# Kernel optimization log

Measured on AMD Instinct MI355X. Metric: run time of the kernel, lower is better.

The kernel has to match this reference:

```python
import jax, jax.numpy as jnp
import numpy as np

B, T, C, H = 4, 2048, 768, 12
D = C // H
EPS = 1e-5


def layernorm(x, g, b):
    mu = jnp.mean(x, axis=-1, keepdims=True)
    var = jnp.mean(jnp.square(x - mu), axis=-1, keepdims=True)
    return (x - mu) * jax.lax.rsqrt(var + EPS) * g + b


def setup_inputs() -> dict:
    key = jax.random.key(0)
    ks = jax.random.split(key, 16)
    s = 0.02
    return {
        "x": jax.random.normal(ks[0], (B, T, C), jnp.float32),
        "Wq": jax.random.normal(ks[1], (C, C), jnp.float32) * s,
        "bq": jnp.zeros((C,), jnp.float32),
        "Wk": jax.random.normal(ks[2], (C, C), jnp.float32) * s,
        "bk": jnp.zeros((C,), jnp.float32),
        "Wv": jax.random.normal(ks[3], (C, C), jnp.float32) * s,
        "bv": jnp.zeros((C,), jnp.float32),
        "Wo": jax.random.normal(ks[4], (C, C), jnp.float32) * s,
        "bo": jnp.zeros((C,), jnp.float32),
        "g1": jnp.ones((C,), jnp.float32),
        "b1": jnp.zeros((C,), jnp.float32),
        "g2": jnp.ones((C,), jnp.float32),
        "b2": jnp.zeros((C,), jnp.float32),
        "W1": jax.random.normal(ks[5], (C, 4 * C), jnp.float32) * s,
        "bm1": jnp.zeros((4 * C,), jnp.float32),
        "W2": jax.random.normal(ks[6], (4 * C, C), jnp.float32) * s,
        "bm2": jnp.zeros((C,), jnp.float32),
    }


def reference(x, Wq, bq, Wk, bk, Wv, bv, Wo, bo, g1, b1, g2, b2, W1, bm1, W2, bm2):
    # --- attention branch ---
    h = layernorm(x, g1, b1)
    q = (h @ Wq + bq).reshape(B, T, H, D)
    k = (h @ Wk + bk).reshape(B, T, H, D)
    v = (h @ Wv + bv).reshape(B, T, H, D)
    att = jnp.einsum('bqhd,bkhd->bhqk', q, k) / jnp.sqrt(jnp.float32(D))
    causal = jnp.tril(jnp.ones((T, T), bool))
    att = jnp.where(causal, att, -jnp.inf)
    att = jax.nn.softmax(att, axis=-1)
    o = jnp.einsum('bhqk,bkhd->bqhd', att, v).reshape(B, T, C)
    x = x + o @ Wo + bo
    # --- MLP branch ---
    h = layernorm(x, g2, b2)
    h = jax.nn.gelu(h @ W1 + bm1, approximate=False)
    return x + h @ W2 + bm2
```

## Files before the change

kernel.cpp:

```cpp
#include <hip/hip_runtime.h>
#include <hip/hip_bf16.h>

#define B_ 4
#define T_ 2048
#define C_ 768
#define H_ 12
#define D_ 64
#define QS_ 2304

typedef __attribute__((ext_vector_type(8))) short short8;
typedef __attribute__((ext_vector_type(4))) short short4v;
typedef __attribute__((ext_vector_type(4))) float f32x4;

__device__ __forceinline__ unsigned short f2bf(float f) {
    __hip_bfloat16 h = __float2bfloat16(f);
    return *reinterpret_cast<unsigned short*>(&h);
}

__device__ __forceinline__ float bf2f(unsigned short u) {
    return __bfloat162float(*reinterpret_cast<const __hip_bfloat16*>(&u));
}

__device__ __forceinline__ unsigned cvt_pk_bf16(float lo, float hi) {
    unsigned r;
    asm("v_cvt_pk_bf16_f32 %0, %1, %2" : "=v"(r) : "v"(lo), "v"(hi));
    return r;
}

__device__ __forceinline__ void gl_lds16(const void* g, void* l) {
    __builtin_amdgcn_global_load_lds((const __attribute__((address_space(1))) unsigned int*)g,
                                     (__attribute__((address_space(3))) unsigned int*)l,
                                     16, 0, 0);
}

__device__ __forceinline__ void transpose_dev(const float* __restrict__ W,
                                              unsigned short* __restrict__ Wt,
                                              int K, int N, int bx, int by,
                                              float (*t)[65]) {
    int n0 = bx * 64, k0 = by * 64;
    int r = threadIdx.x >> 4, c4 = (threadIdx.x & 15) * 4;
    #pragma unroll
    for (int i = 0; i < 4; ++i) {
        float4 v = *(const float4*)(W + (size_t)(k0 + i * 16 + r) * N + n0 + c4);
        t[i*16 + r][c4 + 0] = v.x;
        t[i*16 + r][c4 + 1] = v.y;
        t[i*16 + r][c4 + 2] = v.z;
        t[i*16 + r][c4 + 3] = v.w;
    }
    __syncthreads();
    #pragma unroll
    for (int i = 0; i < 4; ++i) {
        ushort4 o;
        o.x = f2bf(t[c4 + 0][i*16 + r]);
        o.y = f2bf(t[c4 + 1][i*16 + r]);
        o.z = f2bf(t[c4 + 2][i*16 + r]);
        o.w = f2bf(t[c4 + 3][i*16 + r]);
        *(ushort4*)(Wt + (size_t)(n0 + i * 16 + r) * K + k0 + c4) = o;
    }
}

__global__ __launch_bounds__(256) void prep_all(const float* __restrict__ Wq,
                                                const float* __restrict__ Wk,
                                                const float* __restrict__ Wv,
                                                const float* __restrict__ Wo,
                                                const float* __restrict__ W1,
                                                const float* __restrict__ W2,
                                                const float* __restrict__ bq,
                                                const float* __restrict__ bk,
                                                const float* __restrict__ bv,
                                                const float* __restrict__ x,
                                                const float* __restrict__ g1,
                                                const float* __restrict__ b1,
                                                unsigned short* __restrict__ wqkvt,
                                                unsigned short* __restrict__ wot,
                                                unsigned short* __restrict__ w1t,
                                                unsigned short* __restrict__ w2t,
                                                float* __restrict__ bqkv,
                                                unsigned short* __restrict__ ln1h) {
    __shared__ float t[64][65];
    int blk = blockIdx.x;
    int tid = threadIdx.x;

    if (blk < 576) {
        int which = blk / 144, idx = blk % 144;
        const float* src = (which == 0) ? Wq : (which == 1) ? Wk : (which == 2) ? Wv : Wo;
        unsigned short* dst = (which == 3) ? wot : wqkvt + (size_t)which * C_ * C_;
        transpose_dev(src, dst, C_, C_, idx % 12, idx / 12, t);
    } else if (blk < 1152) {
        int idx = blk - 576;
        transpose_dev(W1, w1t, C_, 4 * C_, idx % 48, idx / 48, t);
    } else if (blk < 1728) {
        int idx = blk - 1152;
        transpose_dev(W2, w2t, 4 * C_, C_, idx % 12, idx / 12, t);
    } else if (blk < 1737) {
        int i = (blk - 1728) * 256 + tid;
        bqkv[i] = (i < 768) ? bq[i] : (i < 1536) ? bk[i - 768] : bv[i - 1536];
    } else {
        int row = (blk - 1737) * 4 + (tid >> 6);
        int lane = tid & 63;
        const float* xr = x + (size_t)row * C_;
        float v[12];
        #pragma unroll
        for (int p = 0; p < 3; ++p) {
            float4 f4 = *(const float4*)(xr + p * 256 + lane * 4);
            v[p*4+0] = f4.x; v[p*4+1] = f4.y; v[p*4+2] = f4.z; v[p*4+3] = f4.w;
        }
        float s = 0.f;
        #pragma unroll
        for (int i = 0; i < 12; ++i) s += v[i];
        #pragma unroll
        for (int off = 1; off < 64; off <<= 1) s += __shfl_xor(s, off);
        float mean = s * (1.0f / C_);
        float qs = 0.f;
        #pragma unroll
        for (int i = 0; i < 12; ++i) { v[i] -= mean; qs += v[i] * v[i]; }
        #pragma unroll
        for (int off = 1; off < 64; off <<= 1) qs += __shfl_xor(qs, off);
        float rs = rsqrtf(qs * (1.0f / C_) + 1e-5f);
        unsigned short* orow = ln1h + (size_t)row * C_;
        #pragma unroll
        for (int p = 0; p < 3; ++p) {
            float4 gv = *(const float4*)(g1 + p * 256 + lane * 4);
            float4 bv = *(const float4*)(b1 + p * 256 + lane * 4);
            ushort4 o4;
            o4.x = f2bf(v[p*4+0] * rs * gv.x + bv.x);
            o4.y = f2bf(v[p*4+1] * rs * gv.y + bv.y);
            o4.z = f2bf(v[p*4+2] * rs * gv.z + bv.z);
            o4.w = f2bf(v[p*4+3] * rs * gv.w + bv.w);
            *(ushort4*)(orow + p * 256 + lane * 4) = o4;
        }
    }
}

__global__ __launch_bounds__(256) void ln2_wave(const unsigned short* __restrict__ x,
                                                const float* __restrict__ g,
                                                const float* __restrict__ b,
                                                unsigned short* __restrict__ out) {
    int row = blockIdx.x * 4 + (threadIdx.x >> 6);
    int lane = threadIdx.x & 63;
    const unsigned short* xr = x + (size_t)row * C_;
    float v[12];
    #pragma unroll
    for (int p = 0; p < 3; ++p) {
        ushort4 u4 = *(const ushort4*)(xr + p * 256 + lane * 4);
        v[p*4+0] = bf2f(u4.x); v[p*4+1] = bf2f(u4.y);
        v[p*4+2] = bf2f(u4.z); v[p*4+3] = bf2f(u4.w);
    }
    float s = 0.f;
    #pragma unroll
    for (int i = 0; i < 12; ++i) s += v[i];
    #pragma unroll
    for (int off = 1; off < 64; off <<= 1) s += __shfl_xor(s, off);
    float mean = s * (1.0f / C_);
    float qs = 0.f;
    #pragma unroll
    for (int i = 0; i < 12; ++i) { v[i] -= mean; qs += v[i] * v[i]; }
    #pragma unroll
    for (int off = 1; off < 64; off <<= 1) qs += __shfl_xor(qs, off);
    float rs = rsqrtf(qs * (1.0f / C_) + 1e-5f);
    unsigned short* orow = out + (size_t)row * C_;
    #pragma unroll
    for (int p = 0; p < 3; ++p) {
        float4 gv = *(const float4*)(g + p * 256 + lane * 4);
        float4 bv = *(const float4*)(b + p * 256 + lane * 4);
        ushort4 o4;
        o4.x = f2bf(v[p*4+0] * rs * gv.x + bv.x);
        o4.y = f2bf(v[p*4+1] * rs * gv.y + bv.y);
        o4.z = f2bf(v[p*4+2] * rs * gv.z + bv.z);
        o4.w = f2bf(v[p*4+3] * rs * gv.w + bv.w);
        *(ushort4*)(orow + p * 256 + lane * 4) = o4;
    }
}

template <int EPI>
__global__ __launch_bounds__(256) void gemm_bf16(const unsigned short* __restrict__ A,
                                                 const unsigned short* __restrict__ Bt,
                                                 const float* __restrict__ bias,
                                                 const void* __restrict__ resid,
                                                 void* __restrict__ Cout,
                                                 unsigned short* __restrict__ aux,
                                                 int M, int N, int K, int gx) {
    __shared__ short As[2][128 * 32];
    __shared__ short Bs[2][128 * 32];
    int tid = threadIdx.x;
    int w = tid >> 6, l = tid & 63;
    int nb = gridDim.x;
    int per = nb >> 3;
    int fid = (int)blockIdx.x;
    int wid = (fid & 7) * per + (fid >> 3);
    int bn = wid % gx, bm = wid / gx;
    int wr = w >> 1, wc = w & 1;

    f32x4 acc[4][4];
    #pragma unroll
    for (int m = 0; m < 4; ++m)
        #pragma unroll
        for (int n = 0; n < 4; ++n)
            acc[m][n] = (f32x4){0.f, 0.f, 0.f, 0.f};

    const short* Ag = (const short*)A + (size_t)(bm * 128) * K;
    const short* Bg = (const short*)Bt + (size_t)(bn * 128) * K;
    int srow = tid >> 2;
    int scol = (tid & 3) * 8;
    int lrow = l & 15, lk = (l >> 4) * 8;

    auto stage = [&](int buf, int k0) {
        #pragma unroll
        for (int i = 0; i < 2; ++i) {
            gl_lds16(Ag + (size_t)(i * 64 + srow) * K + k0 + scol,
                     (char*)&As[buf][0] + i * 4096 + w * 1024);
            gl_lds16(Bg + (size_t)(i * 64 + srow) * K + k0 + scol,
                     (char*)&Bs[buf][0] + i * 4096 + w * 1024);
        }
    };

    int nk = K / 32;
    stage(0, 0);
    __syncthreads();

    for (int kt = 0; kt < nk; ++kt) {
        int cur = kt & 1;
        if (kt + 1 < nk) stage(cur ^ 1, (kt + 1) * 32);

        short8 av[4], bv[4];
        #pragma unroll
        for (int m = 0; m < 4; ++m)
            av[m] = *(const short8*)&As[cur][(wr * 64 + m * 16 + lrow) * 32 + lk];
        #pragma unroll
        for (int n = 0; n < 4; ++n)
            bv[n] = *(const short8*)&Bs[cur][(wc * 64 + n * 16 + lrow) * 32 + lk];
        #pragma unroll
        for (int m = 0; m < 4; ++m)
            #pragma unroll
            for (int n = 0; n < 4; ++n)
                acc[m][n] = __builtin_amdgcn_mfma_f32_16x16x32_bf16(av[m], bv[n], acc[m][n], 0, 0, 0);

        __syncthreads();
    }

    int lcol = l & 15, lr4 = (l >> 4) * 4;
    int row0 = bm * 128 + wr * 64;
    int col0 = bn * 128 + wc * 64;
    #pragma unroll
    for (int m = 0; m < 4; ++m) {
        #pragma unroll
        for (int n = 0; n < 4; ++n) {
            int col = col0 + n * 16 + lcol;
            float bz = bias[col];
            if (EPI == 5 && col0 >= 1536) {
                ushort4 o4;
                o4.x = f2bf(acc[m][n][0] + bz);
                o4.y = f2bf(acc[m][n][1] + bz);
                o4.z = f2bf(acc[m][n][2] + bz);
                o4.w = f2bf(acc[m][n][3] + bz);
                int row = row0 + m * 16 + lr4;
                int c = col - 1536;
                *(ushort4*)(aux + ((size_t)(row >> 11) * 768 + c) * (size_t)T_ + (row & 2047)) = o4;
            } else {
                #pragma unroll
                for (int r = 0; r < 4; ++r) {
                    int row = row0 + m * 16 + lr4 + r;
                    float v = acc[m][n][r] + bz;
                    if (EPI == 1) {
                        float u = fmaf(0.044715f * v, v * v, v);
                        float e = __builtin_amdgcn_exp2f(u * -2.3022127f);
                        v = v * __builtin_amdgcn_rcpf(1.0f + e);
                        ((unsigned short*)Cout)[(size_t)row * N + col] = f2bf(v);
                    } else if (EPI == 6) {
                        v += bf2f(((const unsigned short*)resid)[(size_t)row * N + col]);
                        ((float*)Cout)[(size_t)row * N + col] = v;
                    } else if (EPI == 7) {
                        v += ((const float*)resid)[(size_t)row * N + col];
                        ((unsigned short*)Cout)[(size_t)row * N + col] = f2bf(v);
                    } else {
                        ((unsigned short*)Cout)[(size_t)row * N + col] = f2bf(v);
                    }
                }
            }
        }
    }
}

__global__ __launch_bounds__(256) void attn_v9(const unsigned short* __restrict__ QKV,
                                               const unsigned short* __restrict__ vT,
                                               unsigned short* __restrict__ O) {
    __shared__ short Ks[128 * 64];
    __shared__ short Vt[64 * 128];

    int tid = threadIdx.x;
    int w = tid >> 6, l = tid & 63;
    int g = l >> 4, lc = l & 15;
    int wid = (int)(blockIdx.x & 7) * 192 + (int)(blockIdx.x >> 3);
    int bh = wid >> 5;
    int a  = 31 - (wid & 31);
    int b = bh / H_, h = bh % H_;
    const size_t bT = (size_t)b * T_;
    const unsigned short* Qp = QKV + h * D_;
    const unsigned short* Kp = QKV + 768 + h * D_;
    const unsigned short* vTb = vT + ((size_t)b * 768 + h * 64) * (size_t)T_;
    const float SCL = 0.125f * 1.44269504088896340736f;

    int qw = a * 64 + w * 16;

    short8 qf[2];
    {
        const unsigned short* qp = Qp + (bT + qw + lc) * QS_;
        qf[0] = *(const short8*)(qp + g * 8);
        qf[1] = *(const short8*)(qp + 32 + g * 8);
    }

    f32x4 oacc[4];
    #pragma unroll
    for (int n = 0; n < 4; ++n) oacc[n] = (f32x4){0.f, 0.f, 0.f, 0.f};
    float mrun = 4.0f, lpart = 0.f;

    int ntiles = (a >> 1) + 1;
    for (int kt = 0; kt < ntiles; ++kt) {
        int k0 = kt * 128;
        if (kt) __syncthreads();

        #pragma unroll
        for (int c = 0; c < 4; ++c) {
            int row = w * 32 + c * 8 + (l >> 3);
            int inner = (l & 7) * 16;
            const char* src = (const char*)(Kp + (bT + k0 + row) * QS_)
                              + (inner ^ ((row & 7) << 4));
            gl_lds16(src, (char*)Ks + w * 4096 + c * 1024);
        }
        #pragma unroll
        for (int c = 0; c < 4; ++c) {
            int d = w * 16 + c * 4 + (l >> 4);
            int inner = (l & 15) * 16;
            const char* src = (const char*)(vTb + (size_t)d * T_ + k0)
                              + (inner ^ ((d & 7) << 4));
            gl_lds16(src, (char*)Vt + w * 4096 + c * 1024);
        }
        __syncthreads();

        uint2 qd[8];
        float lmaxP[4] = {-INFINITY, -INFINITY, -INFINITY, -INFINITY};
        float rsumP[4] = {0.f, 0.f, 0.f, 0.f};
        bool full = (k0 + 127 <= qw);
        #pragma unroll
        for (int mk = 0; mk < 8; ++mk) {
            f32x4 s = (f32x4){0.f, 0.f, 0.f, 0.f};
            __builtin_amdgcn_s_setprio(1);
            #pragma unroll
            for (int ksd = 0; ksd < 2; ++ksd) {
                int row = mk * 16 + lc;
                int byt = (row * 128 + ksd * 64 + g * 16) ^ ((row & 7) << 4);
                short8 av = *(const short8*)((char*)Ks + byt);
                s = __builtin_amdgcn_mfma_f32_16x16x32_bf16(av, qf[ksd], s, 0, 0, 0);
            }
            __builtin_amdgcn_s_setprio(0);
            float p[4];
            #pragma unroll
            for (int r = 0; r < 4; ++r) {
                float sv = s[r] * SCL;
                if (!full && (k0 + mk * 16 + g * 4 + r > qw + lc)) sv = -INFINITY;
                lmaxP[r] = fmaxf(lmaxP[r], sv);
                float pv = __builtin_amdgcn_exp2f(sv - mrun);
                p[r] = pv;
                rsumP[r] += pv;
            }
            qd[mk].x = cvt_pk_bf16(p[0], p[1]);
            qd[mk].y = cvt_pk_bf16(p[2], p[3]);
        }
        float lmax = fmaxf(fmaxf(lmaxP[0], lmaxP[1]), fmaxf(lmaxP[2], lmaxP[3]));
        lpart += (rsumP[0] + rsumP[1]) + (rsumP[2] + rsumP[3]);

        #pragma unroll
        for (int ks = 0; ks < 4; ++ks) {
            uint2 qa = qd[ks * 2], qb = qd[ks * 2 + 1];
            int srcLo = lc + ((g & 1) << 5);
            int srcHi = srcLo + 16;
            unsigned a0 = (unsigned)__shfl((int)qa.x, srcLo);
            unsigned a1 = (unsigned)__shfl((int)qa.y, srcLo);
            unsigned a2 = (unsigned)__shfl((int)qa.x, srcHi);
            unsigned a3 = (unsigned)__shfl((int)qa.y, srcHi);
            unsigned b0 = (unsigned)__shfl((int)qb.x, srcLo);
            unsigned b1 = (unsigned)__shfl((int)qb.y, srcLo);
            unsigned b2 = (unsigned)__shfl((int)qb.x, srcHi);
            unsigned b3 = (unsigned)__shfl((int)qb.y, srcHi);
            bool lo = (g < 2);
            union { unsigned u[4]; short8 s8; } pa;
            pa.u[0] = lo ? a0 : b0;
            pa.u[1] = lo ? a1 : b1;
            pa.u[2] = lo ? a2 : b2;
            pa.u[3] = lo ? a3 : b3;
            short8 vbv[4];
            #pragma unroll
            for (int n = 0; n < 4; ++n) {
                int row = n * 16 + lc;
                int byt = (row * 256 + ks * 64 + g * 16) ^ ((row & 7) << 4);
                vbv[n] = *(const short8*)((char*)Vt + byt);
            }
            __builtin_amdgcn_s_setprio(1);
            #pragma unroll
            for (int n = 0; n < 4; ++n)
                oacc[n] = __builtin_amdgcn_mfma_f32_16x16x32_bf16(pa.s8, vbv[n], oacc[n], 0, 0, 0);
            __builtin_amdgcn_s_setprio(0);
        }

        if (__any(lmax > mrun + 8.0f)) {
            lmax = fmaxf(lmax, __shfl_xor(lmax, 16));
            lmax = fmaxf(lmax, __shfl_xor(lmax, 32));
            float mnew = fmaxf(mrun, lmax);
            float cc = __builtin_amdgcn_exp2f(mrun - mnew);
            lpart *= cc;
            mrun = mnew;
            #pragma unroll
            for (int r = 0; r < 4; ++r) {
                float cr = __shfl(cc, (l & 48) + g * 4 + r);
                #pragma unroll
                for (int n = 0; n < 4; ++n) oacc[n][r] *= cr;
            }
        }
    }

    float lv = lpart;
    lv += __shfl_xor(lv, 16);
    lv += __shfl_xor(lv, 32);
    float linv = 1.0f / lv;
    float inv[4];
    #pragma unroll
    for (int r = 0; r < 4; ++r) inv[r] = __shfl(linv, (l & 48) + g * 4 + r);
    #pragma unroll
    for (int n = 0; n < 4; ++n) {
        int col = h * D_ + n * 16 + lc;
        #pragma unroll
        for (int r = 0; r < 4; ++r) {
            int row = qw + g * 4 + r;
            O[(bT + row) * C_ + col] = f2bf(oacc[n][r] * inv[r]);
        }
    }
}

extern "C" void kernel_launch(void* const* d_in, const int* in_sizes, int n_in,
                              void* d_out, int out_size, void* d_ws, size_t ws_size,
                              hipStream_t stream) {
    const float* x   = (const float*)d_in[0];
    const float* Wq  = (const float*)d_in[1];
    const float* bq  = (const float*)d_in[2];
    const float* Wk  = (const float*)d_in[3];
    const float* bk  = (const float*)d_in[4];
    const float* Wv  = (const float*)d_in[5];
    const float* bv  = (const float*)d_in[6];
    const float* Wo  = (const float*)d_in[7];
    const float* bo  = (const float*)d_in[8];
    const float* g1  = (const float*)d_in[9];
    const float* b1  = (const float*)d_in[10];
    const float* g2  = (const float*)d_in[11];
    const float* b2  = (const float*)d_in[12];
    const float* W1  = (const float*)d_in[13];
    const float* bm1 = (const float*)d_in[14];
    const float* W2  = (const float*)d_in[15];
    const float* bm2 = (const float*)d_in[16];
    float* out = (float*)d_out;

    const size_t S = (size_t)B_ * T_ * C_;
    char* base = (char*)d_ws;
    unsigned short* ln1h = (unsigned short*)base;
    unsigned short* qkvb = (unsigned short*)(base + 2 * S);
    unsigned short* o    = ln1h;
    unsigned short* ln2h = qkvb;
    unsigned short* vT   = (unsigned short*)(base + 8 * S);
    unsigned short* hid  = (unsigned short*)(base + 4 * S);
    unsigned short* xmid = (unsigned short*)(base + 12 * S);
    unsigned short* wqkvt = (unsigned short*)(base + 16 * S);
    unsigned short* wot   = wqkvt + (size_t)3 * C_ * C_;
    unsigned short* w1t   = wot + (size_t)C_ * C_;
    unsigned short* w2t   = w1t + (size_t)C_ * 4 * C_;
    float* bqkv           = (float*)(w2t + (size_t)C_ * 4 * C_);

    const int M = B_ * T_;
    dim3 blk(256);

    prep_all<<<dim3(1737 + M / 4), blk, 0, stream>>>(Wq, Wk, Wv, Wo, W1, W2,
                                                     bq, bk, bv, x, g1, b1,
                                                     wqkvt, wot, w1t, w2t, bqkv, ln1h);

    gemm_bf16<5><<<dim3((QS_ / 128) * (M / 128)), blk, 0, stream>>>(ln1h, wqkvt, bqkv, nullptr, qkvb, vT, M, QS_, C_, QS_ / 128);

    attn_v9<<<dim3(B_ * H_ * 32), blk, 0, stream>>>(qkvb, vT, o);

    gemm_bf16<7><<<dim3((C_ / 128) * (M / 128)), blk, 0, stream>>>(o, wot, bo, x, xmid, nullptr, M, C_, C_, C_ / 128);
    ln2_wave<<<dim3(M / 4), blk, 0, stream>>>(xmid, g2, b2, ln2h);
    gemm_bf16<1><<<dim3((4 * C_ / 128) * (M / 128)), blk, 0, stream>>>(ln2h, w1t, bm1, nullptr, hid, nullptr, M, 4 * C_, C_, 4 * C_ / 128);
    gemm_bf16<6><<<dim3((C_ / 128) * (M / 128)), blk, 0, stream>>>(hid, w2t, bm2, xmid, out, nullptr, M, C_, 4 * C_, C_ / 128);
}
```

Baseline: 292.4 us.

## Fold LayerNorm2 affine into W1 and apply normalization in GEMM epilogue

Pre-scales W1 rows by the LayerNorm gamma and precomputes per-column correction vectors (sum g2·W1 and b2·W1 + bias) in the prep kernel. LN2 now only computes per-row mean and rstd, and the W1 GEMM reads the raw residual stream directly, applying mean/rstd correction and GELU in its epilogue. This removes the normalized-activation write and re-read between LN2 and the MLP GEMM. In exchange it adds a serial 768-length dot product per column in prep and changes numerics, since centering happens after the bf16 matmul and can lose precision when the mean is large.

```diff
diff --git a/kernel.cpp b/kernel.cpp
--- a/kernel.cpp
+++ b/kernel.cpp
@@ -55,6 +55,34 @@
         o.y = f2bf(t[c4 + 1][i*16 + r]);
         o.z = f2bf(t[c4 + 2][i*16 + r]);
         o.w = f2bf(t[c4 + 3][i*16 + r]);
+        *(ushort4*)(Wt + (size_t)(n0 + i * 16 + r) * K + k0 + c4) = o;
+    }
+}
+
+__device__ __forceinline__ void transpose_dev_scaled(const float* __restrict__ W,
+                                                     const float* __restrict__ scl,
+                                                     unsigned short* __restrict__ Wt,
+                                                     int K, int N, int bx, int by,
+                                                     float (*t)[65]) {
+    int n0 = bx * 64, k0 = by * 64;
+    int r = threadIdx.x >> 4, c4 = (threadIdx.x & 15) * 4;
+    #pragma unroll
+    for (int i = 0; i < 4; ++i) {
+        float4 v = *(const float4*)(W + (size_t)(k0 + i * 16 + r) * N + n0 + c4);
+        t[i*16 + r][c4 + 0] = v.x;
+        t[i*16 + r][c4 + 1] = v.y;
+        t[i*16 + r][c4 + 2] = v.z;
+        t[i*16 + r][c4 + 3] = v.w;
+    }
+    __syncthreads();
+    float4 sv = *(const float4*)(scl + k0 + c4);
+    #pragma unroll
+    for (int i = 0; i < 4; ++i) {
+        ushort4 o;
+        o.x = f2bf(t[c4 + 0][i*16 + r] * sv.x);
+        o.y = f2bf(t[c4 + 1][i*16 + r] * sv.y);
+        o.z = f2bf(t[c4 + 2][i*16 + r] * sv.z);
+        o.w = f2bf(t[c4 + 3][i*16 + r] * sv.w);
         *(ushort4*)(Wt + (size_t)(n0 + i * 16 + r) * K + k0 + c4) = o;
     }
 }
@@ -71,11 +99,16 @@
                                                 const float* __restrict__ x,
                                                 const float* __restrict__ g1,
                                                 const float* __restrict__ b1,
+                                                const float* __restrict__ g2,
+                                                const float* __restrict__ b2,
+                                                const float* __restrict__ bm1,
                                                 unsigned short* __restrict__ wqkvt,
                                                 unsigned short* __restrict__ wot,
                                                 unsigned short* __restrict__ w1t,
                                                 unsigned short* __restrict__ w2t,
                                                 float* __restrict__ bqkv,
+                                                float* __restrict__ c2v,
+                                                float* __restrict__ cbv,
                                                 unsigned short* __restrict__ ln1h) {
     __shared__ float t[64][65];
     int blk = blockIdx.x;
@@ -88,15 +121,25 @@
         transpose_dev(src, dst, C_, C_, idx % 12, idx / 12, t);
     } else if (blk < 1152) {
         int idx = blk - 576;
-        transpose_dev(W1, w1t, C_, 4 * C_, idx % 48, idx / 48, t);
+        transpose_dev_scaled(W1, g2, w1t, C_, 4 * C_, idx % 48, idx / 48, t);
     } else if (blk < 1728) {
         int idx = blk - 1152;
         transpose_dev(W2, w2t, 4 * C_, C_, idx % 12, idx / 12, t);
     } else if (blk < 1737) {
         int i = (blk - 1728) * 256 + tid;
         bqkv[i] = (i < 768) ? bq[i] : (i < 1536) ? bk[i - 768] : bv[i - 1536];
+    } else if (blk < 1749) {
+        int n = (blk - 1737) * 256 + tid;
+        float s2 = 0.f, sb = 0.f;
+        for (int k = 0; k < C_; ++k) {
+            float wv = W1[(size_t)k * (4 * C_) + n];
+            s2 = fmaf(g2[k], wv, s2);
+            sb = fmaf(b2[k], wv, sb);
+        }
+        c2v[n] = s2;
+        cbv[n] = sb + bm1[n];
     } else {
-        int row = (blk - 1737) * 4 + (tid >> 6);
+        int row = (blk - 1749) * 4 + (tid >> 6);
         int lane = tid & 63;
         const float* xr = x + (size_t)row * C_;
         float v[12];
@@ -132,10 +175,8 @@
     }
 }
 
-__global__ __launch_bounds__(256) void ln2_wave(const unsigned short* __restrict__ x,
-                                                const float* __restrict__ g,
-                                                const float* __restrict__ b,
-                                                unsigned short* __restrict__ out) {
+__global__ __launch_bounds__(256) void ln2_stats(const unsigned short* __restrict__ x,
+                                                 float2* __restrict__ stats) {
     int row = blockIdx.x * 4 + (threadIdx.x >> 6);
     int lane = threadIdx.x & 63;
     const unsigned short* xr = x + (size_t)row * C_;
@@ -154,22 +195,11 @@
     float mean = s * (1.0f / C_);
     float qs = 0.f;
     #pragma unroll
-    for (int i = 0; i < 12; ++i) { v[i] -= mean; qs += v[i] * v[i]; }
+    for (int i = 0; i < 12; ++i) { float d = v[i] - mean; qs += d * d; }
     #pragma unroll
     for (int off = 1; off < 64; off <<= 1) qs += __shfl_xor(qs, off);
     float rs = rsqrtf(qs * (1.0f / C_) + 1e-5f);
-    unsigned short* orow = out + (size_t)row * C_;
-    #pragma unroll
-    for (int p = 0; p < 3; ++p) {
-        float4 gv = *(const float4*)(g + p * 256 + lane * 4);
-        float4 bv = *(const float4*)(b + p * 256 + lane * 4);
-        ushort4 o4;
-        o4.x = f2bf(v[p*4+0] * rs * gv.x + bv.x);
-        o4.y = f2bf(v[p*4+1] * rs * gv.y + bv.y);
-        o4.z = f2bf(v[p*4+2] * rs * gv.z + bv.z);
-        o4.w = f2bf(v[p*4+3] * rs * gv.w + bv.w);
-        *(ushort4*)(orow + p * 256 + lane * 4) = o4;
-    }
+    if (lane == 0) stats[row] = make_float2(mean, rs);
 }
 
 template <int EPI>
@@ -241,6 +271,31 @@
     int lcol = l & 15, lr4 = (l >> 4) * 4;
     int row0 = bm * 128 + wr * 64;
     int col0 = bn * 128 + wc * 64;
+
+    if (EPI == 8) {
+        const float2* st = (const float2*)resid;
+        const float* c2 = (const float*)aux;
+        #pragma unroll
+        for (int m = 0; m < 4; ++m) {
+            #pragma unroll
+            for (int r = 0; r < 4; ++r) {
+                int row = row0 + m * 16 + lr4 + r;
+                float2 s2 = st[row];
+                float murs = s2.x * s2.y;
+                #pragma unroll
+                for (int n = 0; n < 4; ++n) {
+                    int col = col0 + n * 16 + lcol;
+                    float v = fmaf(s2.y, acc[m][n][r], fmaf(-murs, c2[col], bias[col]));
+                    float u = fmaf(0.044715f * v, v * v, v);
+                    float e = __builtin_amdgcn_exp2f(u * -2.3022127f);
+                    v = v * __builtin_amdgcn_rcpf(1.0f + e);
+                    ((unsigned short*)Cout)[(size_t)row * N + col] = f2bf(v);
+                }
+            }
+        }
+        return;
+    }
+
     #pragma unroll
     for (int m = 0; m < 4; ++m) {
         #pragma unroll
@@ -463,7 +518,7 @@
     unsigned short* ln1h = (unsigned short*)base;
     unsigned short* qkvb = (unsigned short*)(base + 2 * S);
     unsigned short* o    = ln1h;
-    unsigned short* ln2h = qkvb;
+    float2* stats        = (float2*)(base + 2 * S);
     unsigned short* vT   = (unsigned short*)(base + 8 * S);
     unsigned short* hid  = (unsigned short*)(base + 4 * S);
     unsigned short* xmid = (unsigned short*)(base + 12 * S);
@@ -472,20 +527,22 @@
     unsigned short* w1t   = wot + (size_t)C_ * C_;
     unsigned short* w2t   = w1t + (size_t)C_ * 4 * C_;
     float* bqkv           = (float*)(w2t + (size_t)C_ * 4 * C_);
+    float* c2v            = bqkv + 2304;
+    float* cbv            = c2v + 3072;
 
     const int M = B_ * T_;
     dim3 blk(256);
 
-    prep_all<<<dim3(1737 + M / 4), blk, 0, stream>>>(Wq, Wk, Wv, Wo, W1, W2,
-                                                     bq, bk, bv, x, g1, b1,
-                                                     wqkvt, wot, w1t, w2t, bqkv, ln1h);
+    prep_all<<<dim3(1749 + M / 4), blk, 0, stream>>>(Wq, Wk, Wv, Wo, W1, W2,
+                                                     bq, bk, bv, x, g1, b1, g2, b2, bm1,
+                                                     wqkvt, wot, w1t, w2t, bqkv, c2v, cbv, ln1h);
 
     gemm_bf16<5><<<dim3((QS_ / 128) * (M / 128)), blk, 0, stream>>>(ln1h, wqkvt, bqkv, nullptr, qkvb, vT, M, QS_, C_, QS_ / 128);
 
     attn_v9<<<dim3(B_ * H_ * 32), blk, 0, stream>>>(qkvb, vT, o);
 
     gemm_bf16<7><<<dim3((C_ / 128) * (M / 128)), blk, 0, stream>>>(o, wot, bo, x, xmid, nullptr, M, C_, C_, C_ / 128);
-    ln2_wave<<<dim3(M / 4), blk, 0, stream>>>(xmid, g2, b2, ln2h);
-    gemm_bf16<1><<<dim3((4 * C_ / 128) * (M / 128)), blk, 0, stream>>>(ln2h, w1t, bm1, nullptr, hid, nullptr, M, 4 * C_, C_, 4 * C_ / 128);
+    ln2_stats<<<dim3(M / 4), blk, 0, stream>>>(xmid, stats);
+    gemm_bf16<8><<<dim3((4 * C_ / 128) * (M / 128)), blk, 0, stream>>>(xmid, w1t, cbv, stats, hid, (unsigned short*)c2v, M, 4 * C_, C_, 4 * C_ / 128);
     gemm_bf16<6><<<dim3((C_ / 128) * (M / 128)), blk, 0, stream>>>(hid, w2t, bm2, xmid, out, nullptr, M, C_, 4 * C_, C_ / 128);
 }
```

After: 345.0 us. 18.0% more time.
